# Kernel tuning notes

Measured on AMD Instinct MI355X. Metric: run time of the kernel, lower is better.

Reference implementation:

```python
import jax, jax.numpy as jnp
import numpy as np
from jax import lax

N, S, K, V, C, D, NH, NB, HD = 4, 1024, 4, 32000, 1000, 512, 8, 6, 2048
DH = D // NH
CAP = round((S // K) * 1.0)  # expert capacity = Seq//K * capacity_factor


def setup_inputs() -> dict:
    key = jax.random.key(0)
    ks = jax.random.split(key, 12)
    nrm = lambda k, shape: jax.random.normal(k, shape, dtype=jnp.float32) * 0.02
    return dict(
        x_in=jax.random.randint(ks[0], (N, S), 0, V),
        y_target=jax.random.randint(ks[1], (N, S), 0, C),
        tok_emb=nrm(ks[2], (K, V, D)),
        pos_emb=nrm(ks[3], (K, S, D)),
        ln1_s=jnp.ones((K, NB, D)), ln1_b=jnp.zeros((K, NB, D)),
        Wqkv=nrm(ks[4], (K, NB, D, 3 * D)), bqkv=jnp.zeros((K, NB, 3 * D)),
        Wo=nrm(ks[5], (K, NB, D, D)), bo=jnp.zeros((K, NB, D)),
        ln2_s=jnp.ones((K, NB, D)), ln2_b=jnp.zeros((K, NB, D)),
        W1=nrm(ks[6], (K, NB, D, HD)), b1=jnp.zeros((K, NB, HD)),
        W2=nrm(ks[7], (K, NB, HD, D)), b2=jnp.zeros((K, NB, D)),
        lnf_s=jnp.ones((K, D)), lnf_b=jnp.zeros((K, D)),
        Wcls=nrm(ks[8], (K, D, C)), bcls=jnp.zeros((K, C)),
        Wconf=nrm(ks[9], (K, D, 1)), bconf=jnp.zeros((K, 1)),
    )


def _ln(x, s, b):
    m = x.mean(-1, keepdims=True)
    v = jnp.var(x, axis=-1, keepdims=True)
    return (x - m) * lax.rsqrt(v + 1e-5) * s + b


def reference(x_in, y_target, tok_emb, pos_emb, ln1_s, ln1_b, Wqkv, bqkv, Wo, bo,
              ln2_s, ln2_b, W1, b1, W2, b2, lnf_s, lnf_b, Wcls, bcls, Wconf, bconf):
    causal = jnp.tril(jnp.ones((S, S), dtype=bool))

    def model_fwd(te, pe, l1s, l1b, wqkv, bq, wo, bo_, l2s, l2b, w1, b1_, w2, b2_, lfs, lfb, wc, bc, wcf, bcf):
        x = te[x_in] + pe[None]  # [N,S,D]
        for i in range(NB):
            h = _ln(x, l1s[i], l1b[i])
            qkv = h @ wqkv[i] + bq[i]
            q, k, v = jnp.split(qkv, 3, axis=-1)
            q = q.reshape(N, S, NH, DH); k = k.reshape(N, S, NH, DH); v = v.reshape(N, S, NH, DH)
            att = jnp.einsum('nqhd,nkhd->nhqk', q, k) / np.float32(np.sqrt(DH))
            att = jax.nn.softmax(jnp.where(causal, att, jnp.float32(-1e9)), axis=-1)
            o = jnp.einsum('nhqk,nkhd->nqhd', att, v).reshape(N, S, D)
            x = x + o @ wo[i] + bo_[i]
            h = _ln(x, l2s[i], l2b[i])
            x = x + jax.nn.gelu(h @ w1[i] + b1_[i]) @ w2[i] + b2_[i]
        x = _ln(x, lfs, lfb)
        return x @ wc + bc, x @ wcf + bcf  # logits [N,S,C], confidence [N,S,1]

    clf, conf = jax.vmap(model_fwd)(tok_emb, pos_emb, ln1_s, ln1_b, Wqkv, bqkv, Wo, bo,
                                    ln2_s, ln2_b, W1, b1, W2, b2, lnf_s, lnf_b, Wcls, bcls, Wconf, bconf)
    combined_classifier = jnp.transpose(clf, (1, 0, 2, 3))       # [N,K,S,C]
    combined_confidence = jnp.transpose(conf[..., 0], (1, 0, 2))  # [N,K,S]

    # --- capacity-constrained auction routing on detached logits ---
    logp = jax.nn.log_softmax(lax.stop_gradient(combined_classifier), axis=-1)
    tgt = jnp.broadcast_to(y_target[:, None, :, None], (N, K, S, 1))
    loss = -jnp.take_along_axis(logp, tgt, axis=-1)[..., 0]  # per-token CE, [N,K,S]
    order = jnp.argsort(loss, axis=1, stable=True)            # [N,K,S] models sorted by loss
    order_s = jnp.transpose(order, (2, 0, 1))                 # [S,N,K]
    rows = jnp.arange(N)

    def step(tc, chunk):  # tc: token_count [N,K]; chunk: [N,K]
        tcm = jnp.take_along_axis(tc, chunk, axis=1)
        best = jnp.argmax((tcm < CAP).astype(jnp.float32), axis=1)
        chosen = chunk[rows, best]
        return tc.at[rows, chosen].add(1.0), chosen

    _, chosen = lax.scan(step, jnp.zeros((N, K), dtype=jnp.float32), order_s)
    activated_models_indices = chosen.T  # [N,S]

    mask = jax.nn.one_hot(activated_models_indices, K, dtype=combined_classifier.dtype)  # [N,S,K]
    mask = jnp.transpose(mask, (0, 2, 1))[..., None]  # [N,K,S,1]
    out = (combined_classifier * mask).sum(axis=1)    # [N,S,C]
    return out, combined_confidence, activated_models_indices
```

## Files before the change

kernel.cpp:

```cpp
#include <hip/hip_runtime.h>
#include <hip/hip_bf16.h>

#define N_  4
#define S_  1024
#define K_  4
#define V_  32000
#define C_  1000
#define D_  512
#define NH_ 8
#define NB_ 6
#define HD_ 2048
#define DH_ 64
#define CAP_ 256
#define M_  (N_*S_)

typedef __attribute__((ext_vector_type(8))) short short8_t;
typedef __attribute__((ext_vector_type(4))) float f32x4_t;

#define MFMA16(a,b,c) __builtin_amdgcn_mfma_f32_16x16x32_bf16((a),(b),(c),0,0,0)

#define HSPLANE ((size_t)M_ * D_)
#define WTMAX   ((size_t)524288)

static __device__ __forceinline__ float bfround(float v) {
    unsigned u = __float_as_uint(v);
    u = (u + 0x7FFFu + ((u >> 16) & 1u)) & 0xFFFF0000u;
    return __uint_as_float(u);
}
static __device__ __forceinline__ void split3(float v, unsigned short& a, unsigned short& b, unsigned short& c) {
    const float f0 = bfround(v);      const float r1 = v - f0;
    const float f1 = bfround(r1);     const float f2 = bfround(r1 - f1);
    a = (unsigned short)(__float_as_uint(f0) >> 16);
    b = (unsigned short)(__float_as_uint(f1) >> 16);
    c = (unsigned short)(__float_as_uint(f2) >> 16);
}
static __device__ __forceinline__ float b2f(unsigned short u) {
    return __uint_as_float((unsigned)u << 16);
}

__global__ __launch_bounds__(256) void embed_kernel(const int* __restrict__ x_in,
    const float* __restrict__ tok, const float* __restrict__ pos, float* __restrict__ x)
{
    const int idx = blockIdx.x * 256 + threadIdx.x;
    const int total = M_ * (D_ / 4);
    if (idx >= total) return;
    const int d = (idx & (D_ / 4 - 1)) * 4;
    const int row = idx >> 7;
    const int s = row & (S_ - 1);
    const int t = x_in[row];
    const float4 a = *(const float4*)(tok + (size_t)t * D_ + d);
    const float4 b = *(const float4*)(pos + (size_t)s * D_ + d);
    float4 r; r.x = a.x + b.x; r.y = a.y + b.y; r.z = a.z + b.z; r.w = a.w + b.w;
    *(float4*)(x + (size_t)row * D_ + d) = r;
}

__global__ __launch_bounds__(256) void ln_kernel(const float* __restrict__ x,
    const float* __restrict__ sc, const float* __restrict__ bi, unsigned short* __restrict__ hs)
{
    const int row = blockIdx.x, tid = threadIdx.x;
    const float* xr = x + (size_t)row * D_;
    float v0 = xr[tid], v1 = xr[tid + 256];
    float s1 = v0 + v1;
#pragma unroll
    for (int off = 32; off; off >>= 1) s1 += __shfl_down(s1, off, 64);
    __shared__ float red[8];
    __shared__ float stat[2];
    const int wid = tid >> 6, lane = tid & 63;
    if (lane == 0) red[wid] = s1;
    __syncthreads();
    if (tid == 0) stat[0] = (red[0] + red[1] + red[2] + red[3]) * (1.f / (float)D_);
    __syncthreads();
    const float mean = stat[0];
    const float d0 = v0 - mean, d1 = v1 - mean;
    float s2 = d0 * d0 + d1 * d1;
#pragma unroll
    for (int off = 32; off; off >>= 1) s2 += __shfl_down(s2, off, 64);
    if (lane == 0) red[wid] = s2;
    __syncthreads();
    if (tid == 0) stat[1] = (red[0] + red[1] + red[2] + red[3]) * (1.f / (float)D_);
    __syncthreads();
    const float rstd = rsqrtf(stat[1] + 1e-5f);
    const float o0 = d0 * rstd * sc[tid] + bi[tid];
    const float o1 = d1 * rstd * sc[tid + 256] + bi[tid + 256];
    unsigned short a, b, c;
    const size_t base = (size_t)row * D_ + tid;
    split3(o0, a, b, c);
    hs[base] = a; hs[base + HSPLANE] = b; hs[base + 2 * HSPLANE] = c;
    split3(o1, a, b, c);
    hs[base + 256] = a; hs[base + 256 + HSPLANE] = b; hs[base + 256 + 2 * HSPLANE] = c;
}

__global__ __launch_bounds__(256) void wsplit_kernel(const float* __restrict__ W, int ldw, int NcTrue,
    unsigned short* __restrict__ Wt, size_t bplane, int Kd)
{
    const int tid = threadIdx.x;
    const int n = blockIdx.x * 64 + (tid & 63);
    const int k0 = blockIdx.y * 32 + (tid >> 6) * 8;
    unsigned short q0[8], q1[8], q2[8];
    if (n < NcTrue) {
#pragma unroll
        for (int j = 0; j < 8; ++j) split3(W[(size_t)(k0 + j) * ldw + n], q0[j], q1[j], q2[j]);
    } else {
#pragma unroll
        for (int j = 0; j < 8; ++j) { q0[j] = 0; q1[j] = 0; q2[j] = 0; }
    }
    unsigned short* dst = Wt + (size_t)n * Kd + k0;
    *(uint4*)dst = *(uint4*)&q0[0];
    *(uint4*)(dst + bplane) = *(uint4*)&q1[0];
    *(uint4*)(dst + 2 * bplane) = *(uint4*)&q2[0];
}

template<int MODE>
__global__ __launch_bounds__(256, 2) void gemm64(const unsigned short* __restrict__ A3, size_t aplane,
    const unsigned short* __restrict__ Bt, size_t bplane, const float* __restrict__ bias,
    void* __restrict__ Cv, size_t cplane, int Nc, int ldc)
{
    constexpr int KD = (MODE == 4) ? 1024 : 512;
    __shared__ __align__(16) unsigned short Bs[3][64][40];
    const int tid = threadIdx.x;
    const int bm = blockIdx.y * 128, bn = blockIdx.x * 64;
    const int wid = tid >> 6, lane = tid & 63;
    const int wm = (wid >> 1) * 64, wn = (wid & 1) * 32;
    const int lr = lane & 15, lg = lane >> 4;
    const int scol = tid >> 2, skq = tid & 3;
    const unsigned short* Bp0 = Bt + (size_t)(bn + scol) * KD + skq * 8;
    const unsigned short* Ap0 = A3 + (size_t)(bm + wm + lr) * KD + lg * 8;

    f32x4_t acc[4][2] = {};

#pragma unroll
    for (int k0 = 0; k0 < KD; k0 += 32) {
        const uint4 bq0 = *(const uint4*)(Bp0 + k0);
        const uint4 bq1 = *(const uint4*)(Bp0 + bplane + k0);
        const uint4 bq2 = *(const uint4*)(Bp0 + 2 * bplane + k0);
        short8_t af[3][4];
#pragma unroll
        for (int m = 0; m < 4; ++m) {
            const unsigned short* ap = Ap0 + (size_t)m * 16 * KD + k0;
            af[0][m] = *(const short8_t*)ap;
            af[1][m] = *(const short8_t*)(ap + aplane);
            af[2][m] = *(const short8_t*)(ap + 2 * aplane);
        }
        __syncthreads();
        *(uint4*)&Bs[0][scol][skq * 8] = bq0;
        *(uint4*)&Bs[1][scol][skq * 8] = bq1;
        *(uint4*)&Bs[2][scol][skq * 8] = bq2;
        __syncthreads();
        short8_t bg[3][2];
#pragma unroll
        for (int s = 0; s < 3; ++s)
#pragma unroll
            for (int n2 = 0; n2 < 2; ++n2)
                bg[s][n2] = *(const short8_t*)&Bs[s][wn + n2 * 16 + lr][lg * 8];
#pragma unroll
        for (int m = 0; m < 4; ++m)
#pragma unroll
            for (int n2 = 0; n2 < 2; ++n2) {
                f32x4_t c = acc[m][n2];
                c = MFMA16(af[0][m], bg[0][n2], c);
                c = MFMA16(af[0][m], bg[1][n2], c);
                c = MFMA16(af[1][m], bg[0][n2], c);
                c = MFMA16(af[1][m], bg[1][n2], c);
                c = MFMA16(af[0][m], bg[2][n2], c);
                c = MFMA16(af[2][m], bg[0][n2], c);
                acc[m][n2] = c;
            }
    }
#pragma unroll
    for (int m = 0; m < 4; ++m)
#pragma unroll
        for (int n2 = 0; n2 < 2; ++n2) {
            const int col = bn + wn + n2 * 16 + lr;
            if (col >= Nc) continue;
            const float bv = bias ? bias[col] : 0.f;
            const int row0 = bm + wm + m * 16 + lg * 4;
#pragma unroll
            for (int r = 0; r < 4; ++r) {
                float v = acc[m][n2][r] + bv;
                if (MODE == 2) {
                    const float t = v;
                    v = 0.5f * t * (1.f + tanhf(0.7978845608028654f * (t + 0.044715f * t * t * t)));
                    unsigned short a, b, c;
                    split3(v, a, b, c);
                    unsigned short* Cp = (unsigned short*)Cv + (size_t)(row0 + r) * ldc + col;
                    Cp[0] = a; Cp[cplane] = b; Cp[2 * cplane] = c;
                } else {
                    float* cp = (float*)Cv + (size_t)(row0 + r) * ldc + col;
                    if (MODE == 1 || MODE == 4) v += *cp;
                    *cp = v;
                }
            }
        }
}

__global__ __launch_bounds__(256) void rerun_kernel(const unsigned short* __restrict__ A,
    const unsigned short* __restrict__ B0, const float* __restrict__ bias,
    const int* __restrict__ chosen, const int kk, float* __restrict__ out)
{
    __shared__ int anyrow;
    const int tid = threadIdx.x;
    const int bm = blockIdx.y * 128, bn = blockIdx.x * 64;
    if (tid == 0) anyrow = 0;
    __syncthreads();
    if (tid < 128 && chosen[bm + tid] == kk) anyrow = 1;
    __syncthreads();
    if (!anyrow) return;
    const int wid = tid >> 6, lane = tid & 63;
    const int wm = (wid >> 1) * 64, wn = (wid & 1) * 32;
    const int lr = lane & 15, lg = lane >> 4;
    f32x4_t acc[4][2] = {};
#pragma unroll
    for (int k0 = 0; k0 < D_; k0 += 32) {
        short8_t af[4], bg[2];
#pragma unroll
        for (int m = 0; m < 4; ++m)
            af[m] = *(const short8_t*)(A + (size_t)(bm + wm + m * 16 + lr) * D_ + k0 + lg * 8);
#pragma unroll
        for (int n2 = 0; n2 < 2; ++n2)
            bg[n2] = *(const short8_t*)(B0 + (size_t)(bn + wn + n2 * 16 + lr) * D_ + k0 + lg * 8);
#pragma unroll
        for (int m = 0; m < 4; ++m)
#pragma unroll
            for (int n2 = 0; n2 < 2; ++n2)
                acc[m][n2] = MFMA16(af[m], bg[n2], acc[m][n2]);
    }
#pragma unroll
    for (int m = 0; m < 4; ++m)
#pragma unroll
        for (int n2 = 0; n2 < 2; ++n2) {
            const int col = bn + wn + n2 * 16 + lr;
            if (col >= C_) continue;
            const float bv = bias[col];
            const int row0 = bm + wm + m * 16 + lg * 4;
#pragma unroll
            for (int r = 0; r < 4; ++r) {
                const int row = row0 + r;
                if (chosen[row] == kk) out[(size_t)row * C_ + col] = acc[m][n2][r] + bv;
            }
        }
}

__global__ __launch_bounds__(256) void attn_mfma_kernel(const float* __restrict__ qkv, unsigned short* __restrict__ hsO)
{
    __shared__ __align__(16) unsigned short Ks[3][32][72];
    __shared__ __align__(16) unsigned short Vt[3][64][40];
    __shared__ __align__(16) unsigned short Ps[4][3][16][40];
    const int qt = blockIdx.x, hh = blockIdx.y, n = blockIdx.z;
    const int tid = threadIdx.x;
    const int w = tid >> 6, lane = tid & 63;
    const int lr = lane & 15, lg = lane >> 4;
    const size_t rs = 3 * D_;
    const float* base = qkv + (size_t)n * S_ * rs + hh * DH_;

    short8_t qf[3][2];
    {
        const int qrow = qt * 64 + w * 16 + lr;
#pragma unroll
        for (int ks = 0; ks < 2; ++ks) {
            const float* qp = base + (size_t)qrow * rs + ks * 32 + lg * 8;
            float v[8];
            *(float4*)&v[0] = ((const float4*)qp)[0];
            *(float4*)&v[4] = ((const float4*)qp)[1];
#pragma unroll
            for (int j = 0; j < 8; ++j) {
                unsigned short a, b, c;
                split3(v[j], a, b, c);
                qf[0][ks][j] = (short)a; qf[1][ks][j] = (short)b; qf[2][ks][j] = (short)c;
            }
        }
    }

    f32x4_t oacc[4] = {};
    float m_r[4], l_r[4];
#pragma unroll
    for (int r = 0; r < 4; ++r) { m_r[r] = -1e30f; l_r[r] = 0.f; }

    const int ktmax = 2 * qt + 2;
    for (int kt = 0; kt < ktmax; ++kt) {
        __syncthreads();
        {
            const int key = tid & 31, seg = tid >> 5;
            const float* kp = base + (size_t)(kt * 32 + key) * rs + D_ + seg * 8;
            const float* vp = kp + D_;
            float kv[8], vv[8];
            *(float4*)&kv[0] = ((const float4*)kp)[0];
            *(float4*)&kv[4] = ((const float4*)kp)[1];
            *(float4*)&vv[0] = ((const float4*)vp)[0];
            *(float4*)&vv[4] = ((const float4*)vp)[1];
            unsigned short k0a[8], k1a[8], k2a[8];
#pragma unroll
            for (int j = 0; j < 8; ++j) split3(kv[j], k0a[j], k1a[j], k2a[j]);
            *(uint4*)&Ks[0][key][seg * 8] = *(uint4*)&k0a[0];
            *(uint4*)&Ks[1][key][seg * 8] = *(uint4*)&k1a[0];
            *(uint4*)&Ks[2][key][seg * 8] = *(uint4*)&k2a[0];
#pragma unroll
            for (int j = 0; j < 8; ++j) {
                unsigned short a, b, c;
                split3(vv[j], a, b, c);
                Vt[0][seg * 8 + j][key] = a;
                Vt[1][seg * 8 + j][key] = b;
                Vt[2][seg * 8 + j][key] = c;
            }
        }
        __syncthreads();
        f32x4_t sacc[2] = {};
#pragma unroll
        for (int n2 = 0; n2 < 2; ++n2) {
#pragma unroll
            for (int ks = 0; ks < 2; ++ks) {
                short8_t kb0 = *(const short8_t*)&Ks[0][n2 * 16 + lr][ks * 32 + lg * 8];
                short8_t kb1 = *(const short8_t*)&Ks[1][n2 * 16 + lr][ks * 32 + lg * 8];
                short8_t kb2 = *(const short8_t*)&Ks[2][n2 * 16 + lr][ks * 32 + lg * 8];
                f32x4_t c = sacc[n2];
                c = MFMA16(qf[0][ks], kb0, c);
                c = MFMA16(qf[0][ks], kb1, c);
                c = MFMA16(qf[1][ks], kb0, c);
                c = MFMA16(qf[1][ks], kb1, c);
                c = MFMA16(qf[0][ks], kb2, c);
                c = MFMA16(qf[2][ks], kb0, c);
                sacc[n2] = c;
            }
        }
        float p[2][4];
#pragma unroll
        for (int n2 = 0; n2 < 2; ++n2)
#pragma unroll
            for (int r = 0; r < 4; ++r) {
                float s = sacc[n2][r] * 0.125f;
                const int key = kt * 32 + n2 * 16 + lr;
                const int qrow = qt * 64 + w * 16 + lg * 4 + r;
                if (key > qrow) s = -1e30f;
                p[n2][r] = s;
            }
        float scl[4];
#pragma unroll
        for (int r = 0; r < 4; ++r) {
            float tm = fmaxf(p[0][r], p[1][r]);
            tm = fmaxf(tm, __shfl_xor(tm, 1));
            tm = fmaxf(tm, __shfl_xor(tm, 2));
            tm = fmaxf(tm, __shfl_xor(tm, 4));
            tm = fmaxf(tm, __shfl_xor(tm, 8));
            const float mnew = fmaxf(m_r[r], tm);
            scl[r] = expf(m_r[r] - mnew);
            m_r[r] = mnew;
        }
#pragma unroll
        for (int r = 0; r < 4; ++r) {
            p[0][r] = expf(p[0][r] - m_r[r]);
            p[1][r] = expf(p[1][r] - m_r[r]);
            float ts = p[0][r] + p[1][r];
            ts += __shfl_xor(ts, 1);
            ts += __shfl_xor(ts, 2);
            ts += __shfl_xor(ts, 4);
            ts += __shfl_xor(ts, 8);
            l_r[r] = l_r[r] * scl[r] + ts;
        }
#pragma unroll
        for (int nf = 0; nf < 4; ++nf)
#pragma unroll
            for (int r = 0; r < 4; ++r) oacc[nf][r] *= scl[r];
#pragma unroll
        for (int n2 = 0; n2 < 2; ++n2)
#pragma unroll
            for (int r = 0; r < 4; ++r) {
                unsigned short a, b, c;
                split3(p[n2][r], a, b, c);
                Ps[w][0][lg * 4 + r][n2 * 16 + lr] = a;
                Ps[w][1][lg * 4 + r][n2 * 16 + lr] = b;
                Ps[w][2][lg * 4 + r][n2 * 16 + lr] = c;
            }
        short8_t pa0 = *(const short8_t*)&Ps[w][0][lr][lg * 8];
        short8_t pa1 = *(const short8_t*)&Ps[w][1][lr][lg * 8];
        short8_t pa2 = *(const short8_t*)&Ps[w][2][lr][lg * 8];
#pragma unroll
        for (int nf = 0; nf < 4; ++nf) {
            short8_t vb0 = *(const short8_t*)&Vt[0][nf * 16 + lr][lg * 8];
            short8_t vb1 = *(const short8_t*)&Vt[1][nf * 16 + lr][lg * 8];
            short8_t vb2 = *(const short8_t*)&Vt[2][nf * 16 + lr][lg * 8];
            f32x4_t c = oacc[nf];
            c = MFMA16(pa0, vb0, c);
            c = MFMA16(pa0, vb1, c);
            c = MFMA16(pa1, vb0, c);
            c = MFMA16(pa1, vb1, c);
            c = MFMA16(pa0, vb2, c);
            c = MFMA16(pa2, vb0, c);
            oacc[nf] = c;
        }
    }
    float inv[4];
#pragma unroll
    for (int r = 0; r < 4; ++r) inv[r] = 1.f / l_r[r];
#pragma unroll
    for (int nf = 0; nf < 4; ++nf)
#pragma unroll
        for (int r = 0; r < 4; ++r) {
            const int qrow = qt * 64 + w * 16 + lg * 4 + r;
            const size_t idx = ((size_t)n * S_ + qrow) * D_ + hh * DH_ + nf * 16 + lr;
            unsigned short a, b, c;
            split3(oacc[nf][r] * inv[r], a, b, c);
            hsO[idx] = a; hsO[idx + HSPLANE] = b; hsO[idx + 2 * HSPLANE] = c;
        }
}

__global__ __launch_bounds__(256) void copy_kernel(const unsigned short* __restrict__ src,
    unsigned short* __restrict__ dst)
{
    const int idx = blockIdx.x * 256 + threadIdx.x;
    if (idx >= M_ * D_ / 8) return;
    ((uint4*)dst)[idx] = ((const uint4*)src)[idx];
}

__global__ __launch_bounds__(256) void conf_kernel(const unsigned short* __restrict__ hs,
    const float* __restrict__ w, const float* __restrict__ bc, float* __restrict__ conf_out, int k)
{
    const int wid = threadIdx.x >> 6, lane = threadIdx.x & 63;
    const int row = blockIdx.x * 4 + wid;
    const unsigned short* h0 = hs + (size_t)row * D_;
    const unsigned short* h1 = h0 + HSPLANE;
    float sm = 0.f;
#pragma unroll
    for (int j = 0; j < 8; ++j) {
        const int i = lane + 64 * j;
        sm += (b2f(h0[i]) + b2f(h1[i])) * w[i];
    }
#pragma unroll
    for (int off = 32; off; off >>= 1) sm += __shfl_down(sm, off, 64);
    if (lane == 0) {
        const int n = row >> 10, s = row & (S_ - 1);
        conf_out[((size_t)n * K_ + k) * S_ + s] = sm + bc[0];
    }
}

__global__ __launch_bounds__(256) void loss_kernel(const float* __restrict__ logits,
    const int* __restrict__ y, float* __restrict__ loss)
{
    const int row = blockIdx.x;
    const float* lr = logits + (size_t)row * C_;
    const int tid = threadIdx.x;
    __shared__ float red[256];
    float mx = -1e30f;
    for (int c = tid; c < C_; c += 256) mx = fmaxf(mx, lr[c]);
    red[tid] = mx; __syncthreads();
    for (int st = 128; st > 0; st >>= 1) {
        if (tid < st) red[tid] = fmaxf(red[tid], red[tid + st]);
        __syncthreads();
    }
    mx = red[0];
    __syncthreads();
    float sm = 0.f;
    for (int c = tid; c < C_; c += 256) sm += expf(lr[c] - mx);
    red[tid] = sm; __syncthreads();
    for (int st = 128; st > 0; st >>= 1) {
        if (tid < st) red[tid] += red[tid + st];
        __syncthreads();
    }
    if (tid == 0) loss[row] = logf(red[0]) + mx - lr[y[row]];
}

__global__ __launch_bounds__(256) void routing_kernel(const float* __restrict__ loss,
    float* __restrict__ idx_out, int* __restrict__ chosen_buf)
{
    __shared__ float l_s[K_][S_];
    __shared__ unsigned char ord_s[S_];
    const int n = blockIdx.x;
    const int tid = threadIdx.x;
#pragma unroll
    for (int k = 0; k < K_; ++k)
        ((float4*)l_s[k])[tid] = ((const float4*)(loss + (size_t)k * M_ + n * S_))[tid];
    __syncthreads();
    for (int s = tid; s < S_; s += 256) {
        float l[K_];
#pragma unroll
        for (int k = 0; k < K_; ++k) l[k] = l_s[k][s];
        int ord[K_] = {0, 1, 2, 3};
#pragma unroll
        for (int i = 1; i < K_; ++i) {
            const int v = ord[i];
            int j = i;
            while (j > 0 && l[ord[j - 1]] > l[v]) { ord[j] = ord[j - 1]; --j; }
            ord[j] = v;
        }
        ord_s[s] = (unsigned char)(ord[0] | (ord[1] << 2) | (ord[2] << 4) | (ord[3] << 6));
    }
    __syncthreads();
    if (tid == 0) {
        int tc[K_] = {0, 0, 0, 0};
        for (int s = 0; s < S_; ++s) {
            const unsigned b = ord_s[s];
            int ch = b & 3;
#pragma unroll
            for (int j = 0; j < K_; ++j) {
                const int m = (b >> (2 * j)) & 3;
                if (tc[m] < CAP_) { ch = m; break; }
            }
            ++tc[ch];
            chosen_buf[n * S_ + s] = ch;
            idx_out[n * S_ + s] = (float)ch;
        }
    }
}

extern "C" void kernel_launch(void* const* d_in, const int* in_sizes, int n_in,
                              void* d_out, int out_size, void* d_ws, size_t ws_size,
                              hipStream_t stream)
{
    const int*   x_in = (const int*)d_in[0];
    const int*   y    = (const int*)d_in[1];
    const float* tok  = (const float*)d_in[2];
    const float* pos  = (const float*)d_in[3];
    const float* ln1s = (const float*)d_in[4];
    const float* ln1b = (const float*)d_in[5];
    const float* Wqkv = (const float*)d_in[6];
    const float* bqkv = (const float*)d_in[7];
    const float* Wo   = (const float*)d_in[8];
    const float* bo   = (const float*)d_in[9];
    const float* ln2s = (const float*)d_in[10];
    const float* ln2b = (const float*)d_in[11];
    const float* W1   = (const float*)d_in[12];
    const float* b1   = (const float*)d_in[13];
    const float* W2   = (const float*)d_in[14];
    const float* b2   = (const float*)d_in[15];
    const float* lnfs = (const float*)d_in[16];
    const float* lnfb = (const float*)d_in[17];
    const float* Wcls = (const float*)d_in[18];
    const float* bcls = (const float*)d_in[19];
    const float* Wcnf = (const float*)d_in[20];
    const float* bcnf = (const float*)d_in[21];

    if (ws_size < 66142208) return;
    float* R = (float*)d_ws;
    unsigned short* hs   = (unsigned short*)(R + (size_t)M_ * 1536);
    float* x             = (float*)(hs + 3 * HSPLANE);
    unsigned short* hfin = (unsigned short*)(x + (size_t)M_ * D_);
    unsigned short* Wt   = hfin + (size_t)K_ * M_ * D_;
    float* loss          = (float*)(Wt + 3 * WTMAX);
    int*   chosen        = (int*)(loss + (size_t)K_ * M_);
    unsigned short* mids = (unsigned short*)R;
    const size_t midplane = (size_t)M_ * 1024;

    float* out      = (float*)d_out;
    float* conf_out = out + (size_t)M_ * C_;
    float* idx_out  = conf_out + (size_t)N_ * K_ * S_;

    for (int k = 0; k < K_; ++k) {
        embed_kernel<<<(M_ * (D_ / 4) + 255) / 256, 256, 0, stream>>>(
            x_in, tok + (size_t)k * V_ * D_, pos + (size_t)k * S_ * D_, x);
        for (int i = 0; i < NB_; ++i) {
            const size_t ki = (size_t)k * NB_ + i;
            ln_kernel<<<M_, 256, 0, stream>>>(x, ln1s + ki * D_, ln1b + ki * D_, hs);
            for (int c = 0; c < 2; ++c) {
                wsplit_kernel<<<dim3(12, 16), 256, 0, stream>>>(
                    Wqkv + ki * D_ * 3 * D_ + c * 768, 3 * D_, 768, Wt, 768 * 512, D_);
                gemm64<0><<<dim3(12, 32), 256, 0, stream>>>(
                    hs, HSPLANE, Wt, 768 * 512, bqkv + ki * 3 * D_ + c * 768,
                    R + c * 768, 0, 768, 3 * D_);
            }
            attn_mfma_kernel<<<dim3(S_ / 64, NH_, N_), 256, 0, stream>>>(R, hs);
            wsplit_kernel<<<dim3(8, 16), 256, 0, stream>>>(Wo + ki * D_ * D_, D_, D_, Wt, 512 * 512, D_);
            gemm64<1><<<dim3(8, 32), 256, 0, stream>>>(
                hs, HSPLANE, Wt, 512 * 512, bo + ki * D_, x, 0, D_, D_);
            ln_kernel<<<M_, 256, 0, stream>>>(x, ln2s + ki * D_, ln2b + ki * D_, hs);
            for (int c = 0; c < 2; ++c) {
                wsplit_kernel<<<dim3(16, 16), 256, 0, stream>>>(
                    W1 + ki * D_ * HD_ + c * 1024, HD_, 1024, Wt, 1024 * 512, D_);
                gemm64<2><<<dim3(16, 32), 256, 0, stream>>>(
                    hs, HSPLANE, Wt, 1024 * 512, b1 + ki * HD_ + c * 1024,
                    mids, midplane, 1024, 1024);
                wsplit_kernel<<<dim3(8, 32), 256, 0, stream>>>(
                    W2 + ki * HD_ * D_ + (size_t)c * 1024 * D_, D_, D_, Wt, 512 * 1024, 1024);
                gemm64<4><<<dim3(8, 32), 256, 0, stream>>>(
                    mids, midplane, Wt, 512 * 1024, (c == 0) ? (b2 + ki * D_) : nullptr,
                    x, 0, D_, D_);
            }
        }
        ln_kernel<<<M_, 256, 0, stream>>>(x, lnfs + (size_t)k * D_, lnfb + (size_t)k * D_, hs);
        copy_kernel<<<(M_ * D_ / 8 + 255) / 256, 256, 0, stream>>>(hs, hfin + (size_t)k * M_ * D_);
        wsplit_kernel<<<dim3(16, 16), 256, 0, stream>>>(
            Wcls + (size_t)k * D_ * C_, C_, C_, Wt, 1024 * 512, D_);
        gemm64<0><<<dim3(16, 32), 256, 0, stream>>>(
            hs, HSPLANE, Wt, 1024 * 512, bcls + (size_t)k * C_, R, 0, C_, C_);
        conf_kernel<<<M_ / 4, 256, 0, stream>>>(hs, Wcnf + (size_t)k * D_, bcnf + k, conf_out, k);
        loss_kernel<<<M_, 256, 0, stream>>>(R, y, loss + (size_t)k * M_);
    }
    routing_kernel<<<N_, 256, 0, stream>>>(loss, idx_out, chosen);
    for (int k = 0; k < K_; ++k) {
        wsplit_kernel<<<dim3(16, 16), 256, 0, stream>>>(
            Wcls + (size_t)k * D_ * C_, C_, C_, Wt, 1024 * 512, D_);
        rerun_kernel<<<dim3(16, 32), 256, 0, stream>>>(
            hfin + (size_t)k * M_ * D_, Wt, bcls + (size_t)k * C_, chosen, k, out);
    }
}
```

Before: 13.77 ms.

## Widen GEMM tile to 128x128 and stage A and B through shared memory

The split-bf16 GEMM now uses 128x128 output tiles, with A and B both staged through LDS. It runs the six precision-split product terms as separate passes over K, each with a single-plane A/B pair, instead of loading three planes per k-step. This aims to raise data reuse per LDS load and cut redundant global A loads, since A was previously read straight from global memory by each wave. In exchange, grids have half as many blocks (as few as 128 blocks for the narrower GEMMs), each block has more accumulator registers, and A/B tiles are re-read once per segment.

```diff
diff --git a/kernel.cpp b/kernel.cpp
--- a/kernel.cpp
+++ b/kernel.cpp
@@ -111,72 +111,62 @@
 }
 
 template<int MODE>
-__global__ __launch_bounds__(256, 2) void gemm64(const unsigned short* __restrict__ A3, size_t aplane,
+__global__ __launch_bounds__(256, 2) void gemm128(const unsigned short* __restrict__ A3, size_t aplane,
     const unsigned short* __restrict__ Bt, size_t bplane, const float* __restrict__ bias,
     void* __restrict__ Cv, size_t cplane, int Nc, int ldc)
 {
     constexpr int KD = (MODE == 4) ? 1024 : 512;
-    __shared__ __align__(16) unsigned short Bs[3][64][40];
+    __shared__ __align__(16) unsigned short As[128][40];
+    __shared__ __align__(16) unsigned short Bs[128][40];
     const int tid = threadIdx.x;
-    const int bm = blockIdx.y * 128, bn = blockIdx.x * 64;
+    const int bm = blockIdx.y * 128, bn = blockIdx.x * 128;
     const int wid = tid >> 6, lane = tid & 63;
-    const int wm = (wid >> 1) * 64, wn = (wid & 1) * 32;
+    const int wm = (wid >> 1) * 64, wn = (wid & 1) * 64;
     const int lr = lane & 15, lg = lane >> 4;
-    const int scol = tid >> 2, skq = tid & 3;
-    const unsigned short* Bp0 = Bt + (size_t)(bn + scol) * KD + skq * 8;
-    const unsigned short* Ap0 = A3 + (size_t)(bm + wm + lr) * KD + lg * 8;
-
-    f32x4_t acc[4][2] = {};
-
-#pragma unroll
-    for (int k0 = 0; k0 < KD; k0 += 32) {
-        const uint4 bq0 = *(const uint4*)(Bp0 + k0);
-        const uint4 bq1 = *(const uint4*)(Bp0 + bplane + k0);
-        const uint4 bq2 = *(const uint4*)(Bp0 + 2 * bplane + k0);
-        short8_t af[3][4];
-#pragma unroll
-        for (int m = 0; m < 4; ++m) {
-            const unsigned short* ap = Ap0 + (size_t)m * 16 * KD + k0;
-            af[0][m] = *(const short8_t*)ap;
-            af[1][m] = *(const short8_t*)(ap + aplane);
-            af[2][m] = *(const short8_t*)(ap + 2 * aplane);
-        }
-        __syncthreads();
-        *(uint4*)&Bs[0][scol][skq * 8] = bq0;
-        *(uint4*)&Bs[1][scol][skq * 8] = bq1;
-        *(uint4*)&Bs[2][scol][skq * 8] = bq2;
-        __syncthreads();
-        short8_t bg[3][2];
-#pragma unroll
-        for (int s = 0; s < 3; ++s)
-#pragma unroll
-            for (int n2 = 0; n2 < 2; ++n2)
-                bg[s][n2] = *(const short8_t*)&Bs[s][wn + n2 * 16 + lr][lg * 8];
-#pragma unroll
-        for (int m = 0; m < 4; ++m)
-#pragma unroll
-            for (int n2 = 0; n2 < 2; ++n2) {
-                f32x4_t c = acc[m][n2];
-                c = MFMA16(af[0][m], bg[0][n2], c);
-                c = MFMA16(af[0][m], bg[1][n2], c);
-                c = MFMA16(af[1][m], bg[0][n2], c);
-                c = MFMA16(af[1][m], bg[1][n2], c);
-                c = MFMA16(af[0][m], bg[2][n2], c);
-                c = MFMA16(af[2][m], bg[0][n2], c);
-                acc[m][n2] = c;
-            }
+    const int srow = tid >> 1, sof = (tid & 1) * 16;
+
+    f32x4_t acc[4][4] = {};
+
+    for (int seg = 0; seg < 6; ++seg) {
+        const int sa = (0x201100 >> (4 * seg)) & 3;
+        const int sb = (0x021010 >> (4 * seg)) & 3;
+        const unsigned short* Ap = A3 + (size_t)sa * aplane + (size_t)(bm + srow) * KD + sof;
+        const unsigned short* Bp = Bt + (size_t)sb * bplane + (size_t)(bn + srow) * KD + sof;
+#pragma unroll 4
+        for (int k0 = 0; k0 < KD; k0 += 32) {
+            const uint4 av0 = *(const uint4*)(Ap + k0);
+            const uint4 av1 = *(const uint4*)(Ap + k0 + 8);
+            const uint4 bv0 = *(const uint4*)(Bp + k0);
+            const uint4 bv1 = *(const uint4*)(Bp + k0 + 8);
+            __syncthreads();
+            *(uint4*)&As[srow][sof]     = av0;
+            *(uint4*)&As[srow][sof + 8] = av1;
+            *(uint4*)&Bs[srow][sof]     = bv0;
+            *(uint4*)&Bs[srow][sof + 8] = bv1;
+            __syncthreads();
+            short8_t af[4], bf[4];
+#pragma unroll
+            for (int m = 0; m < 4; ++m) af[m] = *(const short8_t*)&As[wm + m * 16 + lr][lg * 8];
+#pragma unroll
+            for (int n = 0; n < 4; ++n) bf[n] = *(const short8_t*)&Bs[wn + n * 16 + lr][lg * 8];
+#pragma unroll
+            for (int m = 0; m < 4; ++m)
+#pragma unroll
+                for (int n = 0; n < 4; ++n)
+                    acc[m][n] = MFMA16(af[m], bf[n], acc[m][n]);
+        }
     }
 #pragma unroll
     for (int m = 0; m < 4; ++m)
 #pragma unroll
-        for (int n2 = 0; n2 < 2; ++n2) {
-            const int col = bn + wn + n2 * 16 + lr;
+        for (int n = 0; n < 4; ++n) {
+            const int col = bn + wn + n * 16 + lr;
             if (col >= Nc) continue;
             const float bv = bias ? bias[col] : 0.f;
             const int row0 = bm + wm + m * 16 + lg * 4;
 #pragma unroll
             for (int r = 0; r < 4; ++r) {
-                float v = acc[m][n2][r] + bv;
+                float v = acc[m][n][r] + bv;
                 if (MODE == 2) {
                     const float t = v;
                     v = 0.5f * t * (1.f + tanhf(0.7978845608028654f * (t + 0.044715f * t * t * t)));
@@ -551,24 +541,24 @@
             for (int c = 0; c < 2; ++c) {
                 wsplit_kernel<<<dim3(12, 16), 256, 0, stream>>>(
                     Wqkv + ki * D_ * 3 * D_ + c * 768, 3 * D_, 768, Wt, 768 * 512, D_);
-                gemm64<0><<<dim3(12, 32), 256, 0, stream>>>(
+                gemm128<0><<<dim3(6, 32), 256, 0, stream>>>(
                     hs, HSPLANE, Wt, 768 * 512, bqkv + ki * 3 * D_ + c * 768,
                     R + c * 768, 0, 768, 3 * D_);
             }
             attn_mfma_kernel<<<dim3(S_ / 64, NH_, N_), 256, 0, stream>>>(R, hs);
             wsplit_kernel<<<dim3(8, 16), 256, 0, stream>>>(Wo + ki * D_ * D_, D_, D_, Wt, 512 * 512, D_);
-            gemm64<1><<<dim3(8, 32), 256, 0, stream>>>(
+            gemm128<1><<<dim3(4, 32), 256, 0, stream>>>(
                 hs, HSPLANE, Wt, 512 * 512, bo + ki * D_, x, 0, D_, D_);
             ln_kernel<<<M_, 256, 0, stream>>>(x, ln2s + ki * D_, ln2b + ki * D_, hs);
             for (int c = 0; c < 2; ++c) {
                 wsplit_kernel<<<dim3(16, 16), 256, 0, stream>>>(
                     W1 + ki * D_ * HD_ + c * 1024, HD_, 1024, Wt, 1024 * 512, D_);
-                gemm64<2><<<dim3(16, 32), 256, 0, stream>>>(
+                gemm128<2><<<dim3(8, 32), 256, 0, stream>>>(
                     hs, HSPLANE, Wt, 1024 * 512, b1 + ki * HD_ + c * 1024,
                     mids, midplane, 1024, 1024);
                 wsplit_kernel<<<dim3(8, 32), 256, 0, stream>>>(
                     W2 + ki * HD_ * D_ + (size_t)c * 1024 * D_, D_, D_, Wt, 512 * 1024, 1024);
-                gemm64<4><<<dim3(8, 32), 256, 0, stream>>>(
+                gemm128<4><<<dim3(4, 32), 256, 0, stream>>>(
                     mids, midplane, Wt, 512 * 1024, (c == 0) ? (b2 + ki * D_) : nullptr,
                     x, 0, D_, D_);
             }
@@ -577,7 +567,7 @@
         copy_kernel<<<(M_ * D_ / 8 + 255) / 256, 256, 0, stream>>>(hs, hfin + (size_t)k * M_ * D_);
         wsplit_kernel<<<dim3(16, 16), 256, 0, stream>>>(
             Wcls + (size_t)k * D_ * C_, C_, C_, Wt, 1024 * 512, D_);
-        gemm64<0><<<dim3(16, 32), 256, 0, stream>>>(
+        gemm128<0><<<dim3(8, 32), 256, 0, stream>>>(
             hs, HSPLANE, Wt, 1024 * 512, bcls + (size_t)k * C_, R, 0, C_, C_);
         conf_kernel<<<M_ / 4, 256, 0, stream>>>(hs, Wcnf + (size_t)k * D_, bcnf + k, conf_out, k);
         loss_kernel<<<M_, 256, 0, stream>>>(R, y, loss + (size_t)k * M_);
```

Measured after the change: 20.21 ms. 46.7% more time.
